# Performance work log

Measured on AMD Instinct MI355X. Metric: run time of the kernel, lower is better.

Reference implementation:

```python
import jax, jax.numpy as jnp
import numpy as np

BSZ, M, D, H = 32768, 8, 128, 512

def setup_inputs() -> dict:
    key = jax.random.key(0)
    k1, k2, k3, k4, k5 = jax.random.split(key, 5)
    q_vec = jax.random.normal(k1, (BSZ, D), dtype=jnp.float32)
    k_vec = jax.random.normal(k2, (BSZ, M, D), dtype=jnp.float32)
    v_vec = jax.random.normal(k3, (BSZ, M, D), dtype=jnp.float32)
    # torch nn.Linear weights: [out_features, in_features], kaiming-uniform-ish scale
    W1 = jax.random.normal(k4, (H, 2 * D), dtype=jnp.float32) * (1.0 / np.sqrt(2 * D))
    W2 = jax.random.normal(k5, (1, H), dtype=jnp.float32) * (1.0 / np.sqrt(H))
    return {"q_vec": q_vec, "k_vec": k_vec, "v_vec": v_vec, "W1": W1, "W2": W2}

def reference(q_vec, k_vec, v_vec, W1, W2):
    bsz, m, d = k_vec.shape
    # repeat query along the hop dim and concat with keys -> [bsz, m, 2d]
    q = jnp.broadcast_to(q_vec[:, None, :], (bsz, m, d))
    xx = jnp.concatenate([q, k_vec], axis=-1)
    h = jax.nn.relu(jnp.einsum('bmk,hk->bmh', xx, W1))      # [bsz, m, hidden]
    scores = jnp.einsum('bmh,oh->bmo', h, W2)               # [bsz, m, 1]
    attn = jax.nn.softmax(scores, axis=1)                   # softmax over hops
    return jnp.sum(v_vec * attn, axis=1)                    # [bsz, d]
```

## Files before the change

kernel.cpp:

```cpp
#include <hip/hip_runtime.h>
#include <stdint.h>

typedef float    f32x4 __attribute__((ext_vector_type(4)));
typedef _Float16 f16x8 __attribute__((ext_vector_type(8)));
typedef _Float16 f16x4 __attribute__((ext_vector_type(4)));

#define BSZ  32768
#define MHOP 8
#define DDIM 128
#define HDIM 512
#define BT   8
#define ROWS 64
#define NT   16
#define NBLK 256
#define AQLD 136

#define BAR_LDS() do { \
    asm volatile("s_waitcnt lgkmcnt(0)" ::: "memory"); \
    __builtin_amdgcn_s_barrier(); \
} while (0)

#define DPP_ADD(s, ctrl) ((s) + __int_as_float(__builtin_amdgcn_update_dpp(0, __float_as_int(s), (ctrl), 0xF, 0xF, true)))
#define DPP_MAX(s, ctrl) fmaxf((s), __int_as_float(__builtin_amdgcn_update_dpp(0, __float_as_int(s), (ctrl), 0xF, 0xF, true)))
#define SWZ_ADD(s, pat)  ((s) + __int_as_float(__builtin_amdgcn_ds_swizzle(__float_as_int(s), (pat))))

__global__ void prep_w1(const float* __restrict__ W1,
                        _Float16* __restrict__ W1q, _Float16* __restrict__ W1k) {
    int i = (blockIdx.x * blockDim.x + threadIdx.x) * 4;
    float4 v = *reinterpret_cast<const float4*>(W1 + i);
    f16x4 o;
    o[0]=(_Float16)v.x; o[1]=(_Float16)v.y; o[2]=(_Float16)v.z; o[3]=(_Float16)v.w;
    int h = i >> 8, c = i & 255;
    _Float16* dst = (c < 128) ? (W1q + h * 128 + c) : (W1k + h * 128 + (c - 128));
    *reinterpret_cast<f16x4*>(dst) = o;
}

__device__ __forceinline__ f16x8 cvt_f16x8(float4 x0, float4 x1) {
    f16x8 p;
    p[0]=(_Float16)x0.x; p[1]=(_Float16)x0.y; p[2]=(_Float16)x0.z; p[3]=(_Float16)x0.w;
    p[4]=(_Float16)x1.x; p[5]=(_Float16)x1.y; p[6]=(_Float16)x1.z; p[7]=(_Float16)x1.w;
    return p;
}

__global__ void __launch_bounds__(512, 2) fused_kernel(
    const float* __restrict__ q_vec,
    const float* __restrict__ k_vec,
    const float* __restrict__ v_vec,
    const _Float16* __restrict__ W1q,
    const _Float16* __restrict__ W1k,
    const float* __restrict__ W2,
    float* __restrict__ out)
{
    __shared__ __align__(16) _Float16 w1k_lds[HDIM * DDIM];
    __shared__ __align__(16) _Float16 a_k[ROWS * DDIM];
    __shared__ __align__(16) _Float16 a_q[BT * AQLD];
    __shared__ __align__(16) _Float16 u_lds[HDIM * BT];
    __shared__ __align__(16) float scores_part[8][ROWS];

    const int t  = threadIdx.x;
    const int w  = t >> 6;
    const int l  = t & 63;
    const int lg = l >> 4;
    const int ll = l & 15;
    const long tile0 = (long)blockIdx.x * NT;

    #pragma unroll
    for (int i2 = 0; i2 < 16; ++i2) {
        int cid = i2 * 512 + t;
        int row = cid >> 4, c = cid & 15;
        f16x8 p = *reinterpret_cast<const f16x8*>(W1k + (size_t)cid * 8);
        *reinterpret_cast<f16x8*>(&w1k_lds[row * DDIM + ((c ^ (row & 7)) * 8)]) = p;
    }

    f16x8 w1qf[4][4];
    {
        const _Float16* base = W1q + (size_t)(w * 64 + ll) * DDIM + lg * 8;
        #pragma unroll
        for (int kf = 0; kf < 4; ++kf)
            #pragma unroll
            for (int fc = 0; fc < 4; ++fc)
                w1qf[kf][fc] = *reinterpret_cast<const f16x8*>(
                    base + (size_t)(fc * 16) * DDIM + kf * 32);
    }
    float w2r[4];
    #pragma unroll
    for (int fc = 0; fc < 4; ++fc) w2r[fc] = W2[w * 64 + fc * 16 + ll];

    float4 kr[2][2]; float4 qr[2];
    {
        const long b0p = tile0 * BT;
        const float4* ks = reinterpret_cast<const float4*>(k_vec + b0p * (MHOP * DDIM));
        kr[0][0] = ks[t * 2];         kr[0][1] = ks[t * 2 + 1];
        kr[1][0] = ks[(t + 512) * 2]; kr[1][1] = ks[(t + 512) * 2 + 1];
        if (t < 128) {
            const float4* qs = reinterpret_cast<const float4*>(q_vec + b0p * DDIM);
            qr[0] = qs[t * 2]; qr[1] = qs[t * 2 + 1];
        }
    }

    for (int it = 0; it < NT; ++it) {
        const long b0 = tile0 * BT + (long)it * BT;

        #pragma unroll
        for (int cc = 0; cc < 2; ++cc) {
            int cid = t + cc * 512, row = cid >> 4, c = cid & 15;
            *reinterpret_cast<f16x8*>(&a_k[row * DDIM + ((c ^ (row & 7)) * 8)]) =
                cvt_f16x8(kr[cc][0], kr[cc][1]);
        }
        if (t < 128) {
            int row = t >> 4, c = t & 15;
            *reinterpret_cast<f16x8*>(&a_q[row * AQLD + c * 8]) = cvt_f16x8(qr[0], qr[1]);
        }
        BAR_LDS();

        if (it + 1 < NT) {
            const long bn = b0 + BT;
            const float4* ks = reinterpret_cast<const float4*>(k_vec + bn * (MHOP * DDIM));
            kr[0][0] = ks[t * 2];         kr[0][1] = ks[t * 2 + 1];
            kr[1][0] = ks[(t + 512) * 2]; kr[1][1] = ks[(t + 512) * 2 + 1];
            if (t < 128) {
                const float4* qs = reinterpret_cast<const float4*>(q_vec + bn * DDIM);
                qr[0] = qs[t * 2]; qr[1] = qs[t * 2 + 1];
            }
        }
        float2 vr[8];
        {
            const float* vb = v_vec + (b0 + w) * (MHOP * DDIM) + l * 2;
            #pragma unroll
            for (int m = 0; m < MHOP; ++m)
                vr[m] = *reinterpret_cast<const float2*>(vb + m * DDIM);
        }

        {
            f32x4 accu[4] = {};
            #pragma unroll
            for (int kf = 0; kf < 4; ++kf) {
                const int kk = kf * 32 + lg * 8;
                f16x8 aq = *reinterpret_cast<const f16x8*>(&a_q[(ll & 7) * AQLD + kk]);
                #pragma unroll
                for (int fc = 0; fc < 4; ++fc)
                    accu[fc] = __builtin_amdgcn_mfma_f32_16x16x32_f16(aq, w1qf[kf][fc], accu[fc], 0, 0, 0);
            }
            if (lg < 2) {
                #pragma unroll
                for (int fc = 0; fc < 4; ++fc) {
                    f16x4 up;
                    up[0]=(_Float16)accu[fc][0]; up[1]=(_Float16)accu[fc][1];
                    up[2]=(_Float16)accu[fc][2]; up[3]=(_Float16)accu[fc][3];
                    *reinterpret_cast<f16x4*>(&u_lds[(w * 64 + fc * 16 + ll) * BT + lg * 4]) = up;
                }
            }
        }

        f32x4 acc[4][4] = {};
        #pragma unroll
        for (int kf = 0; kf < 4; ++kf) {
            const int ch = kf * 4 + lg;
            f16x8 bf[4];
            #pragma unroll
            for (int fc = 0; fc < 4; ++fc) {
                int hrow = w * 64 + fc * 16 + ll;
                bf[fc] = *reinterpret_cast<const f16x8*>(
                    &w1k_lds[hrow * DDIM + ((ch ^ (hrow & 7)) * 8)]);
            }
            #pragma unroll
            for (int fr = 0; fr < 4; ++fr) {
                int row = fr * 16 + ll;
                f16x8 af = *reinterpret_cast<const f16x8*>(
                    &a_k[row * DDIM + ((ch ^ (row & 7)) * 8)]);
                #pragma unroll
                for (int fc = 0; fc < 4; ++fc)
                    acc[fr][fc] = __builtin_amdgcn_mfma_f32_16x16x32_f16(af, bf[fc], acc[fr][fc], 0, 0, 0);
            }
        }

        float uf[4][4];
        {
            #pragma unroll
            for (int fc = 0; fc < 4; ++fc) {
                f16x8 urow = *reinterpret_cast<const f16x8*>(
                    &u_lds[(w * 64 + fc * 16 + ll) * BT]);
                #pragma unroll
                for (int fr = 0; fr < 4; ++fr) {
                    float lo = (float)urow[fr * 2];
                    float hi = (float)urow[fr * 2 + 1];
                    uf[fr][fc] = (lg & 2) ? hi : lo;
                }
            }
        }

        #pragma unroll
        for (int fr = 0; fr < 4; ++fr) {
            float sj[4];
            #pragma unroll
            for (int j = 0; j < 4; ++j) {
                float s = 0.f;
                #pragma unroll
                for (int fc = 0; fc < 4; ++fc)
                    s += w2r[fc] * fmaxf(acc[fr][fc][j] + uf[fr][fc], 0.f);
                s = DPP_ADD(s, 0xB1);
                s = DPP_ADD(s, 0x4E);
                s = DPP_ADD(s, 0x141);
                s = DPP_ADD(s, 0x140);
                sj[j] = s;
            }
            if (ll == 0) {
                f32x4 sv; sv[0]=sj[0]; sv[1]=sj[1]; sv[2]=sj[2]; sv[3]=sj[3];
                *reinterpret_cast<f32x4*>(&scores_part[w][fr * 16 + lg * 4]) = sv;
            }
        }
        BAR_LDS();

        float attn;
        {
            const int m = l & 7, g = l >> 3;
            float s = scores_part[g][w * 8 + m];
            s = SWZ_ADD(s, 0x201F);
            s = SWZ_ADD(s, 0x401F);
            s += __shfl_xor(s, 32);
            float mx = s;
            mx = DPP_MAX(mx, 0xB1);
            mx = DPP_MAX(mx, 0x4E);
            mx = DPP_MAX(mx, 0x141);
            float e = __expf(s - mx);
            float sum = e;
            sum = DPP_ADD(sum, 0xB1);
            sum = DPP_ADD(sum, 0x4E);
            sum = DPP_ADD(sum, 0x141);
            attn = e / sum;
        }

        {
            float a0 = 0.f, a1 = 0.f;
            #pragma unroll
            for (int m = 0; m < MHOP; ++m) {
                float at = __shfl(attn, m, 8);
                a0 += at * vr[m].x;
                a1 += at * vr[m].y;
            }
            float2 o; o.x = a0; o.y = a1;
            *reinterpret_cast<float2*>(out + (b0 + w) * DDIM + l * 2) = o;
        }
    }
}

extern "C" void kernel_launch(void* const* d_in, const int* in_sizes, int n_in,
                              void* d_out, int out_size, void* d_ws, size_t ws_size,
                              hipStream_t stream) {
    const float* q  = (const float*)d_in[0];
    const float* k  = (const float*)d_in[1];
    const float* v  = (const float*)d_in[2];
    const float* W1 = (const float*)d_in[3];
    const float* W2 = (const float*)d_in[4];

    _Float16* W1q = (_Float16*)d_ws;
    _Float16* W1k = (_Float16*)((char*)d_ws + 128 * 1024);

    prep_w1<<<(HDIM * 256) / (256 * 4), 256, 0, stream>>>(W1, W1q, W1k);
    fused_kernel<<<NBLK, 512, 0, stream>>>(q, k, v, W1q, W1k, W2, (float*)d_out);
}
```

Before: 81.07 us.

## Stream prepacked W1q fragments from global instead of holding them in registers

Splits weight prep into a W1k conversion kernel and a kernel that packs the W1q half into per-lane MFMA fragment order. The fused kernel now loads those coalesced fragments from global (L2-resident) on every iteration instead of keeping 16 f16x8 fragments live in registers across the loop, which reduces register pressure. The v_vec loads are moved later, after score computation, to shorten their live range. In exchange, each tile iteration does extra global loads, adds their latency to the query MFMA path, and adds one more kernel launch.

```diff
diff --git a/kernel.cpp b/kernel.cpp
--- a/kernel.cpp
+++ b/kernel.cpp
@@ -24,15 +24,30 @@
 #define DPP_MAX(s, ctrl) fmaxf((s), __int_as_float(__builtin_amdgcn_update_dpp(0, __float_as_int(s), (ctrl), 0xF, 0xF, true)))
 #define SWZ_ADD(s, pat)  ((s) + __int_as_float(__builtin_amdgcn_ds_swizzle(__float_as_int(s), (pat))))
 
-__global__ void prep_w1(const float* __restrict__ W1,
-                        _Float16* __restrict__ W1q, _Float16* __restrict__ W1k) {
+__global__ void prep_w1k(const float* __restrict__ W1, _Float16* __restrict__ W1k) {
     int i = (blockIdx.x * blockDim.x + threadIdx.x) * 4;
-    float4 v = *reinterpret_cast<const float4*>(W1 + i);
+    int h = i >> 7, c = i & 127;
+    float4 v = *reinterpret_cast<const float4*>(W1 + (size_t)h * 256 + 128 + c);
     f16x4 o;
     o[0]=(_Float16)v.x; o[1]=(_Float16)v.y; o[2]=(_Float16)v.z; o[3]=(_Float16)v.w;
-    int h = i >> 8, c = i & 255;
-    _Float16* dst = (c < 128) ? (W1q + h * 128 + c) : (W1k + h * 128 + (c - 128));
-    *reinterpret_cast<f16x4*>(dst) = o;
+    *reinterpret_cast<f16x4*>(W1k + (size_t)h * 128 + c) = o;
+}
+
+__global__ void prep_w1q_pack(const float* __restrict__ W1, _Float16* __restrict__ Pq) {
+    int id = blockIdx.x * blockDim.x + threadIdx.x;
+    int l  = id & 63;
+    int fc = (id >> 6) & 3;
+    int kf = (id >> 8) & 3;
+    int w  = id >> 10;
+    int h  = w * 64 + fc * 16 + (l & 15);
+    int k  = kf * 32 + (l >> 4) * 8;
+    const float* s = W1 + (size_t)h * 256 + k;
+    float4 a = *reinterpret_cast<const float4*>(s);
+    float4 b = *reinterpret_cast<const float4*>(s + 4);
+    f16x8 p;
+    p[0]=(_Float16)a.x; p[1]=(_Float16)a.y; p[2]=(_Float16)a.z; p[3]=(_Float16)a.w;
+    p[4]=(_Float16)b.x; p[5]=(_Float16)b.y; p[6]=(_Float16)b.z; p[7]=(_Float16)b.w;
+    *reinterpret_cast<f16x8*>(Pq + (size_t)id * 8) = p;
 }
 
 __device__ __forceinline__ f16x8 cvt_f16x8(float4 x0, float4 x1) {
@@ -46,8 +61,8 @@
     const float* __restrict__ q_vec,
     const float* __restrict__ k_vec,
     const float* __restrict__ v_vec,
-    const _Float16* __restrict__ W1q,
     const _Float16* __restrict__ W1k,
+    const _Float16* __restrict__ Pq,
     const float* __restrict__ W2,
     float* __restrict__ out)
 {
@@ -72,19 +87,11 @@
         *reinterpret_cast<f16x8*>(&w1k_lds[row * DDIM + ((c ^ (row & 7)) * 8)]) = p;
     }
 
-    f16x8 w1qf[4][4];
-    {
-        const _Float16* base = W1q + (size_t)(w * 64 + ll) * DDIM + lg * 8;
-        #pragma unroll
-        for (int kf = 0; kf < 4; ++kf)
-            #pragma unroll
-            for (int fc = 0; fc < 4; ++fc)
-                w1qf[kf][fc] = *reinterpret_cast<const f16x8*>(
-                    base + (size_t)(fc * 16) * DDIM + kf * 32);
-    }
     float w2r[4];
     #pragma unroll
     for (int fc = 0; fc < 4; ++fc) w2r[fc] = W2[w * 64 + fc * 16 + ll];
+
+    const _Float16* pqw = Pq + (size_t)(w * 16) * 512 + l * 8;
 
     float4 kr[2][2]; float4 qr[2];
     {
@@ -123,13 +130,6 @@
                 qr[0] = qs[t * 2]; qr[1] = qs[t * 2 + 1];
             }
         }
-        float2 vr[8];
-        {
-            const float* vb = v_vec + (b0 + w) * (MHOP * DDIM) + l * 2;
-            #pragma unroll
-            for (int m = 0; m < MHOP; ++m)
-                vr[m] = *reinterpret_cast<const float2*>(vb + m * DDIM);
-        }
 
         {
             f32x4 accu[4] = {};
@@ -137,9 +137,12 @@
             for (int kf = 0; kf < 4; ++kf) {
                 const int kk = kf * 32 + lg * 8;
                 f16x8 aq = *reinterpret_cast<const f16x8*>(&a_q[(ll & 7) * AQLD + kk]);
-                #pragma unroll
-                for (int fc = 0; fc < 4; ++fc)
-                    accu[fc] = __builtin_amdgcn_mfma_f32_16x16x32_f16(aq, w1qf[kf][fc], accu[fc], 0, 0, 0);
+                const _Float16* pq_kf = pqw + (size_t)(kf * 4) * 512;
+                #pragma unroll
+                for (int fc = 0; fc < 4; ++fc) {
+                    f16x8 bq = *reinterpret_cast<const f16x8*>(pq_kf + (size_t)fc * 512);
+                    accu[fc] = __builtin_amdgcn_mfma_f32_16x16x32_f16(aq, bq, accu[fc], 0, 0, 0);
+                }
             }
             if (lg < 2) {
                 #pragma unroll
@@ -175,17 +178,15 @@
         }
 
         float uf[4][4];
-        {
-            #pragma unroll
-            for (int fc = 0; fc < 4; ++fc) {
-                f16x8 urow = *reinterpret_cast<const f16x8*>(
-                    &u_lds[(w * 64 + fc * 16 + ll) * BT]);
-                #pragma unroll
-                for (int fr = 0; fr < 4; ++fr) {
-                    float lo = (float)urow[fr * 2];
-                    float hi = (float)urow[fr * 2 + 1];
-                    uf[fr][fc] = (lg & 2) ? hi : lo;
-                }
+        #pragma unroll
+        for (int fc = 0; fc < 4; ++fc) {
+            f16x8 urow = *reinterpret_cast<const f16x8*>(
+                &u_lds[(w * 64 + fc * 16 + ll) * BT]);
+            #pragma unroll
+            for (int fr = 0; fr < 4; ++fr) {
+                float lo = (float)urow[fr * 2];
+                float hi = (float)urow[fr * 2 + 1];
+                uf[fr][fc] = (lg & 2) ? hi : lo;
             }
         }
 
@@ -208,6 +209,14 @@
                 f32x4 sv; sv[0]=sj[0]; sv[1]=sj[1]; sv[2]=sj[2]; sv[3]=sj[3];
                 *reinterpret_cast<f32x4*>(&scores_part[w][fr * 16 + lg * 4]) = sv;
             }
+        }
+
+        float2 vr[8];
+        {
+            const float* vb = v_vec + (b0 + w) * (MHOP * DDIM) + l * 2;
+            #pragma unroll
+            for (int m = 0; m < MHOP; ++m)
+                vr[m] = *reinterpret_cast<const float2*>(vb + m * DDIM);
         }
         BAR_LDS();
 
@@ -253,9 +262,10 @@
     const float* W1 = (const float*)d_in[3];
     const float* W2 = (const float*)d_in[4];
 
-    _Float16* W1q = (_Float16*)d_ws;
-    _Float16* W1k = (_Float16*)((char*)d_ws + 128 * 1024);
-
-    prep_w1<<<(HDIM * 256) / (256 * 4), 256, 0, stream>>>(W1, W1q, W1k);
-    fused_kernel<<<NBLK, 512, 0, stream>>>(q, k, v, W1q, W1k, W2, (float*)d_out);
-}
+    _Float16* W1k = (_Float16*)d_ws;
+    _Float16* Pq  = (_Float16*)((char*)d_ws + 128 * 1024);
+
+    prep_w1k<<<(HDIM * DDIM) / (256 * 4), 256, 0, stream>>>(W1, W1k);
+    prep_w1q_pack<<<8192 / 256, 256, 0, stream>>>(W1, Pq);
+    fused_kernel<<<NBLK, 512, 0, stream>>>(q, k, v, W1k, Pq, W2, (float*)d_out);
+}
```

After: 115.0 us. 1.42x slower.
